# Optimization experiments

Hardware: AMD Instinct MI355X
Metric: run time of the kernel (lower is better)

## Reference

```python
import jax, jax.numpy as jnp
import numpy as np

K = 4          # conv kernel size
DIL = 3        # conv dilation
EPS = 1e-5     # rms eps inside gate kernel
NORM_EPS = 1e-5  # RMSNorm eps for value rms


def setup_inputs() -> dict:
    key = jax.random.key(0)
    ks = jax.random.split(key, 10)
    B, T, G, C, E = 2, 4096, 4, 1024, 1024
    return {
        "embeddings": jax.random.normal(ks[0], (B, T, E), jnp.float32),
        "hidden_states": jax.random.normal(ks[1], (B, T, G, C), jnp.float32),
        "key_w": jax.random.normal(ks[2], (G * C, E), jnp.float32) * 0.02,
        "key_b": jax.random.normal(ks[3], (G * C,), jnp.float32) * 0.02,
        "value_w": jax.random.normal(ks[4], (C, E), jnp.float32) * 0.02,
        "value_b": jax.random.normal(ks[5], (C,), jnp.float32) * 0.02,
        "w_key_norm": jax.random.uniform(ks[6], (G, C), jnp.float32, 0.5, 1.5),
        "w_query_norm": jax.random.uniform(ks[7], (G, C), jnp.float32, 0.5, 1.5),
        "w_norm": jax.random.uniform(ks[8], (G, C), jnp.float32, 0.5, 1.5),
        "conv_weight": jax.random.normal(ks[9], (G * C, K), jnp.float32) * 0.1,
    }


def reference(embeddings, hidden_states, key_w, key_b, value_w, value_b,
              w_key_norm, w_query_norm, w_norm, conv_weight):
    B, T, G, C = hidden_states.shape
    # projections
    k_all = (embeddings @ key_w.T + key_b).reshape(B, T, G, C)     # [B,T,G,C]
    q_all = hidden_states                                          # [B,T,G,C]
    vproj = embeddings @ value_w.T + value_b                       # [B,T,C]

    # gate kernel: per (b,t,g) RMS of key/query + weighted dot -> sign-sqrt-sigmoid gate
    rms_k = jnp.sqrt(jnp.mean(k_all * k_all, axis=-1) + EPS)       # [B,T,G]
    rms_q = jnp.sqrt(jnp.mean(q_all * q_all, axis=-1) + EPS)       # [B,T,G]
    dot = jnp.einsum('btgc,gc,btgc,gc->btg', k_all, w_key_norm, q_all, w_query_norm)
    gate_raw = dot / (rms_k * rms_q) / jnp.sqrt(jnp.float32(C))
    gate = jax.nn.sigmoid(jnp.where(gate_raw >= 0, 1.0, -1.0)
                          * jnp.sqrt(jnp.maximum(jnp.abs(gate_raw), 1e-6)))
    value = vproj[:, :, None, :] * gate[..., None]                 # [B,T,G,C]
    rms_v = jnp.sqrt(jnp.mean(value * value, axis=-1) + NORM_EPS)  # [B,T,G]

    # conv+residual kernel: per-group RMS-norm, dilated depthwise causal conv, SiLU, residual
    normed = value * (w_norm[None, None] / rms_v[..., None])       # [B,T,G,C]
    conv_w = conv_weight.reshape(G, C, K)                          # depthwise weights
    pad = (K - 1) * DIL
    xp = jnp.pad(normed, ((0, 0), (pad, 0), (0, 0), (0, 0)))
    # acc[b,t,g,c] = sum_k normed[b, t-(K-1-k)*DIL, g, c] * conv_w[g,c,k]
    acc = xp[:, 0:T] * conv_w[None, None, :, :, 0]
    for k in range(1, K):
        acc = acc + xp[:, k * DIL: k * DIL + T] * conv_w[None, None, :, :, k]
    acc = acc * jax.nn.sigmoid(acc)  # SiLU activation
    return value + acc
```

## Files before the change

### kernel.cpp

```cpp
#include <hip/hip_runtime.h>
#include <hip/hip_bf16.h>
#include <cstdint>
#include <cstddef>

using bf16 = __hip_bfloat16;

typedef __bf16 bf16x8_t __attribute__((ext_vector_type(8)));
typedef float  f32x4_t  __attribute__((ext_vector_type(4)));

static constexpr int Bb = 2;
static constexpr int Tt = 4096;
static constexpr int Gg = 4;
static constexpr int Cc = 1024;
static constexpr int Mm = Bb * Tt;
static constexpr int GC = Gg * Cc;

__device__ __forceinline__ float bfbits2f(unsigned u) {
  union { unsigned i; float f; } c; c.i = u << 16; return c.f;
}
__device__ __forceinline__ ushort f2bfbits(float v) {
  union { __hip_bfloat16 h; ushort u; } c; c.h = __float2bfloat16(v); return c.u;
}

__device__ __forceinline__ void store_val(bf16* p, float v)  { *p = __float2bfloat16(v); }
__device__ __forceinline__ void store_val(float* p, float v) { *p = v; }

__device__ __forceinline__ void gld_lds16(const ushort* g, ushort* l) {
  __builtin_amdgcn_global_load_lds(
      (const __attribute__((address_space(1))) void*)g,
      (__attribute__((address_space(3))) void*)l, 16, 0, 0);
}

__global__ __launch_bounds__(256)
void cvt_bf16(const float* __restrict__ in, ushort* __restrict__ out, int n4)
{
  const int i = blockIdx.x * 256 + threadIdx.x;
  if (i >= n4) return;
  const float4 v = ((const float4*)in)[i];
  ushort4 o;
  o.x = f2bfbits(v.x); o.y = f2bfbits(v.y);
  o.z = f2bfbits(v.z); o.w = f2bfbits(v.w);
  ((ushort4*)out)[i] = o;
}

__global__ __launch_bounds__(256)
void cvt_split(const float* __restrict__ in, ushort* __restrict__ hi,
               ushort* __restrict__ lo, int n4)
{
  const int i = blockIdx.x * 256 + threadIdx.x;
  if (i >= n4) return;
  const float4 v = ((const float4*)in)[i];
  ushort4 h, l;
  h.x = f2bfbits(v.x); l.x = f2bfbits(v.x - bfbits2f(h.x));
  h.y = f2bfbits(v.y); l.y = f2bfbits(v.y - bfbits2f(h.y));
  h.z = f2bfbits(v.z); l.z = f2bfbits(v.z - bfbits2f(h.z));
  h.w = f2bfbits(v.w); l.w = f2bfbits(v.w - bfbits2f(h.w));
  ((ushort4*)hi)[i] = h;
  ((ushort4*)lo)[i] = l;
}

__global__ __launch_bounds__(256, 4)
void gemm_key_fused(const ushort* __restrict__ embH, const ushort* __restrict__ embL,
                    const ushort* __restrict__ kwH,  const ushort* __restrict__ kwL,
                    const float* __restrict__ key_b, const float* __restrict__ hid,
                    const float* __restrict__ wkn,   const float* __restrict__ wqn,
                    float* __restrict__ k2_part, float* __restrict__ dot_part,
                    float* __restrict__ q2_part)
{
  constexpr int K = Cc;
  __shared__ __align__(16) ushort sA[128 * 64];
  __shared__ __align__(16) ushort sB[128 * 64];

  const int tid  = threadIdx.x;
  const int lane = tid & 63;
  const int wave = tid >> 6;
  const int wm   = wave & 1;
  const int wn   = wave >> 1;
  const int row0 = blockIdx.y * 128;
  const int col0 = blockIdx.x * 128;

  const int srow = tid >> 3;
  const int schk = (tid & 7) ^ (srow & 7);
  const ushort* aBase = (schk < 4) ? embH : embL;
  const ushort* bBase = (schk < 4) ? kwH  : kwL;
  const int selem = (schk & 3) * 8;
  const int wofs  = wave * 512;

  f32x4_t acc[4][4] = {};

  for (int kt = 0; kt < K; kt += 32) {
#pragma unroll
    for (int p = 0; p < 4; ++p) {
      gld_lds16(aBase + (size_t)(row0 + p * 32 + srow) * K + kt + selem,
                sA + p * 2048 + wofs);
      gld_lds16(bBase + (size_t)(col0 + p * 32 + srow) * K + kt + selem,
                sB + p * 2048 + wofs);
    }
    __syncthreads();

    const int cH = (lane >> 4) ^ (lane & 7);
    const int cL = cH ^ 4;

    bf16x8_t afH[4], afL[4], bfH[4], bfL[4];
#pragma unroll
    for (int mi = 0; mi < 4; ++mi) {
      const int r = wm * 64 + mi * 16 + (lane & 15);
      afH[mi] = *(const bf16x8_t*)(sA + r * 64 + cH * 8);
      afL[mi] = *(const bf16x8_t*)(sA + r * 64 + cL * 8);
    }
#pragma unroll
    for (int ni = 0; ni < 4; ++ni) {
      const int r = wn * 64 + ni * 16 + (lane & 15);
      bfH[ni] = *(const bf16x8_t*)(sB + r * 64 + cH * 8);
      bfL[ni] = *(const bf16x8_t*)(sB + r * 64 + cL * 8);
    }
#pragma unroll
    for (int mi = 0; mi < 4; ++mi)
#pragma unroll
      for (int ni = 0; ni < 4; ++ni) {
        acc[mi][ni] = __builtin_amdgcn_mfma_f32_16x16x32_bf16(
            afH[mi], bfH[ni], acc[mi][ni], 0, 0, 0);
        acc[mi][ni] = __builtin_amdgcn_mfma_f32_16x16x32_bf16(
            afH[mi], bfL[ni], acc[mi][ni], 0, 0, 0);
        acc[mi][ni] = __builtin_amdgcn_mfma_f32_16x16x32_bf16(
            afL[mi], bfH[ni], acc[mi][ni], 0, 0, 0);
      }
    __syncthreads();
  }

  const int lrow = lane >> 4;
  const int lcol = lane & 15;
  const int g    = col0 >> 10;

  float s2[4][4] = {};
  float su[4][4] = {};
  float sq[4][4] = {};

#pragma unroll
  for (int ni = 0; ni < 4; ++ni) {
    const int col = col0 + wn * 64 + ni * 16 + lcol;
    const float kb = key_b[col];
    const float ww = wkn[col] * wqn[col];
#pragma unroll
    for (int mi = 0; mi < 4; ++mi) {
      const int rowb = row0 + wm * 64 + mi * 16 + lrow * 4;
#pragma unroll
      for (int r = 0; r < 4; ++r) {
        const float q = hid[(size_t)(rowb + r) * GC + col];
        const float k = acc[mi][ni][r] + kb;
        s2[mi][r] += k * k;
        su[mi][r] += k * ww * q;
        sq[mi][r] += q * q;
      }
    }
  }
#pragma unroll
  for (int off = 1; off < 16; off <<= 1) {
#pragma unroll
    for (int mi = 0; mi < 4; ++mi)
#pragma unroll
      for (int r = 0; r < 4; ++r) {
        s2[mi][r] += __shfl_xor(s2[mi][r], off);
        su[mi][r] += __shfl_xor(su[mi][r], off);
        sq[mi][r] += __shfl_xor(sq[mi][r], off);
      }
  }
  if (lcol == 0) {
#pragma unroll
    for (int mi = 0; mi < 4; ++mi) {
      const int rowb = row0 + wm * 64 + mi * 16 + lrow * 4;
#pragma unroll
      for (int r = 0; r < 4; ++r) {
        atomicAdd(&k2_part[(rowb + r) * Gg + g],  s2[mi][r]);
        atomicAdd(&dot_part[(rowb + r) * Gg + g], su[mi][r]);
        atomicAdd(&q2_part[(rowb + r) * Gg + g],  sq[mi][r]);
      }
    }
  }
}

template <typename OutT>
__global__ __launch_bounds__(256, 4)
void gemm_bt(const ushort* __restrict__ A, const ushort* __restrict__ Bm,
             const float* __restrict__ bias, OutT* __restrict__ C,
             int M, int N, int K)
{
  __shared__ __align__(16) ushort sA[128 * 64];
  __shared__ __align__(16) ushort sB[128 * 64];

  const int tid  = threadIdx.x;
  const int lane = tid & 63;
  const int wave = tid >> 6;
  const int wm   = wave & 1;
  const int wn   = wave >> 1;
  const int row0 = blockIdx.y * 128;
  const int col0 = blockIdx.x * 128;

  const int srow = tid >> 3;
  const int scol = ((tid & 7) ^ (srow & 7)) * 8;
  ushort* aWB = sA + wave * 512;
  ushort* bWB = sB + wave * 512;

  f32x4_t acc[4][4] = {};

  for (int kt = 0; kt < K; kt += 64) {
#pragma unroll
    for (int p = 0; p < 4; ++p) {
      gld_lds16(A  + (size_t)(row0 + p * 32 + srow) * K + kt + scol,
                aWB + p * 2048);
      gld_lds16(Bm + (size_t)(col0 + p * 32 + srow) * K + kt + scol,
                bWB + p * 2048);
    }
    __syncthreads();

#pragma unroll
    for (int ks = 0; ks < 2; ++ks) {
      const int cb = ks * 4 + (lane >> 4);
      const int ce = ((cb ^ (lane & 7)) * 8);
      bf16x8_t af[4], bfr[4];
#pragma unroll
      for (int mi = 0; mi < 4; ++mi) {
        const int r = wm * 64 + mi * 16 + (lane & 15);
        af[mi] = *(const bf16x8_t*)(sA + r * 64 + ce);
      }
#pragma unroll
      for (int ni = 0; ni < 4; ++ni) {
        const int r = wn * 64 + ni * 16 + (lane & 15);
        bfr[ni] = *(const bf16x8_t*)(sB + r * 64 + ce);
      }
#pragma unroll
      for (int mi = 0; mi < 4; ++mi)
#pragma unroll
        for (int ni = 0; ni < 4; ++ni)
          acc[mi][ni] = __builtin_amdgcn_mfma_f32_16x16x32_bf16(
              af[mi], bfr[ni], acc[mi][ni], 0, 0, 0);
    }
    __syncthreads();
  }

  const int lrow = lane >> 4;
  const int lcol = lane & 15;
#pragma unroll
  for (int ni = 0; ni < 4; ++ni) {
    const int col = col0 + wn * 64 + ni * 16 + lcol;
    const float bv = bias[col];
#pragma unroll
    for (int mi = 0; mi < 4; ++mi) {
      const int rowb = row0 + wm * 64 + mi * 16 + lrow * 4;
#pragma unroll
      for (int r = 0; r < 4; ++r)
        store_val(&C[(size_t)(rowb + r) * N + col], acc[mi][ni][r] + bv);
    }
  }
}

__global__ __launch_bounds__(256)
void finalize_kernel(const float* __restrict__ vproj,
                     const float* __restrict__ k2_part,
                     const float* __restrict__ dot_part,
                     const float* __restrict__ q2_part,
                     float* __restrict__ gate_o, float* __restrict__ snorm_o)
{
  const int bt   = blockIdx.x;
  const int tid  = threadIdx.x;
  const int g    = tid >> 6;
  const int lane = tid & 63;

  const float4 v4 = ((const float4*)(vproj + (size_t)bt * Cc))[tid];
  float pv = v4.x * v4.x + v4.y * v4.y + v4.z * v4.z + v4.w * v4.w;
#pragma unroll
  for (int off = 32; off > 0; off >>= 1) pv += __shfl_xor(pv, off);
  __shared__ float wsum[4];
  if (lane == 0) wsum[g] = pv;
  __syncthreads();

  if (lane == 0) {
    const float mv = (wsum[0] + wsum[1] + wsum[2] + wsum[3]) * (1.0f / 1024.0f);
    const float sk = k2_part[bt * Gg + g];
    const float sd = dot_part[bt * Gg + g];
    const float sq = q2_part[bt * Gg + g];
    const float rk = sqrtf(sk * (1.0f / 1024.0f) + 1e-5f);
    const float rq = sqrtf(sq * (1.0f / 1024.0f) + 1e-5f);
    const float graw = sd / (rk * rq) * (1.0f / 32.0f);
    const float sgn = (graw >= 0.f) ? 1.f : -1.f;
    const float gate = 1.f / (1.f + expf(-sgn * sqrtf(fmaxf(fabsf(graw), 1e-6f))));
    const float rv = sqrtf(gate * gate * mv + 1e-5f);
    gate_o[bt * Gg + g]  = gate;
    snorm_o[bt * Gg + g] = gate / rv;
  }
}

static constexpr int CJ  = 128;
static constexpr int NCH = 11;

__global__ __launch_bounds__(256)
void conv_kernel(const float* __restrict__ vproj, const float* __restrict__ gate,
                 const float* __restrict__ snorm, const float* __restrict__ wnm,
                 const float* __restrict__ cw, float* __restrict__ out)
{
  int x = blockIdx.x;
  const int cb = x & 3;  x >>= 2;
  const int p  = x % 3;  x /= 3;
  const int ch = x % NCH; x /= NCH;
  const int g  = x & 3;  x >>= 2;
  const int b  = x;
  const int c  = cb * 256 + threadIdx.x;

  const float wn = wnm[g * Cc + c];
  const float4 w = ((const float4*)cw)[g * Cc + c];

  int t = p + 3 * (ch * CJ);
  if (t >= Tt) return;

  float n1 = 0.f, n2 = 0.f, n3 = 0.f;
#pragma unroll
  for (int h = 3; h >= 1; --h) {
    const int th = t - 3 * h;
    float nv = 0.f;
    if (th >= 0) {
      const int bt = b * Tt + th;
      nv = vproj[(size_t)bt * Cc + c] * snorm[bt * Gg + g] * wn;
    }
    n3 = n2; n2 = n1; n1 = nv;
  }

  for (int j = 0; j < CJ && t < Tt; ++j, t += 3) {
    const int bt = b * Tt + t;
    const float vp  = vproj[(size_t)bt * Cc + c];
    const float gt  = gate[bt * Gg + g];
    const float sn  = snorm[bt * Gg + g];
    const float cur = vp * sn * wn;
    const float a   = w.x * n3 + w.y * n2 + w.z * n1 + w.w * cur;
    const float si  = a / (1.f + __expf(-a));
    out[((size_t)bt * Gg + g) * Cc + c] = vp * gt + si;
    n3 = n2; n2 = n1; n1 = cur;
  }
}

extern "C" void kernel_launch(void* const* d_in, const int* in_sizes, int n_in,
                              void* d_out, int out_size, void* d_ws, size_t ws_size,
                              hipStream_t stream)
{
  const float* emb   = (const float*)d_in[0];
  const float* hid   = (const float*)d_in[1];
  const float* key_w = (const float*)d_in[2];
  const float* key_b = (const float*)d_in[3];
  const float* val_w = (const float*)d_in[4];
  const float* val_b = (const float*)d_in[5];
  const float* wkn   = (const float*)d_in[6];
  const float* wqn   = (const float*)d_in[7];
  const float* wnm   = (const float*)d_in[8];
  const float* cwt   = (const float*)d_in[9];
  float* out = (float*)d_out;

  char* ws = (char*)d_ws;
  ushort* embH  = (ushort*)ws;  ws += (size_t)Mm * Cc * 2;
  ushort* embL  = (ushort*)ws;  ws += (size_t)Mm * Cc * 2;
  ushort* kwH   = (ushort*)ws;  ws += (size_t)GC * Cc * 2;
  ushort* kwL   = (ushort*)ws;  ws += (size_t)GC * Cc * 2;
  ushort* vwB   = (ushort*)ws;  ws += (size_t)Cc * Cc * 2;
  float*  vproj = (float*)ws;   ws += (size_t)Mm * Cc * 4;
  float*  k2p   = (float*)ws;   ws += (size_t)Mm * Gg * 4;
  float*  dotp  = (float*)ws;   ws += (size_t)Mm * Gg * 4;
  float*  q2p   = (float*)ws;   ws += (size_t)Mm * Gg * 4;
  float*  gate  = (float*)ws;   ws += (size_t)Mm * Gg * 4;
  float*  snorm = (float*)ws;

  hipMemsetAsync(k2p, 0, (size_t)3 * Mm * Gg * 4, stream);

  dim3 blk(256);
  cvt_split<<<dim3((Mm * Cc / 4) / 256), blk, 0, stream>>>(emb,   embH, embL, Mm * Cc / 4);
  cvt_split<<<dim3((GC * Cc / 4) / 256), blk, 0, stream>>>(key_w, kwH,  kwL,  GC * Cc / 4);
  cvt_bf16 <<<dim3((Cc * Cc / 4) / 256), blk, 0, stream>>>(val_w, vwB,  Cc * Cc / 4);

  gemm_key_fused<<<dim3(GC / 128, Mm / 128), blk, 0, stream>>>(
      embH, embL, kwH, kwL, key_b, hid, wkn, wqn, k2p, dotp, q2p);

  gemm_bt<float><<<dim3(Cc / 128, Mm / 128), blk, 0, stream>>>(
      embH, vwB, val_b, vproj, Mm, Cc, Cc);

  finalize_kernel<<<dim3(Mm), blk, 0, stream>>>(vproj, k2p, dotp, q2p, gate, snorm);

  const int nblocks = Bb * Gg * NCH * 3 * (Cc / 256);
  conv_kernel<<<dim3(nblocks), blk, 0, stream>>>(vproj, gate, snorm, wnm, cwt, out);
}
```

Baseline: 615.5 us.

## Restructure key GEMM into 256x256 tiles with double-buffered ping-pong pipeline

```diff
diff --git a/kernel.cpp b/kernel.cpp
--- a/kernel.cpp
+++ b/kernel.cpp
@@ -59,7 +59,7 @@
   ((ushort4*)lo)[i] = l;
 }
 
-__global__ __launch_bounds__(256, 4)
+__global__ __launch_bounds__(512, 2)
 void gemm_key_fused(const ushort* __restrict__ embH, const ushort* __restrict__ embL,
                     const ushort* __restrict__ kwH,  const ushort* __restrict__ kwL,
                     const float* __restrict__ key_b, const float* __restrict__ hid,
@@ -67,113 +67,141 @@
                     float* __restrict__ k2_part, float* __restrict__ dot_part,
                     float* __restrict__ q2_part)
 {
-  constexpr int K = Cc;
-  __shared__ __align__(16) ushort sA[128 * 64];
-  __shared__ __align__(16) ushort sB[128 * 64];
+  constexpr int NT = 32;
+  __shared__ __align__(16) ushort sA[2 * 16384];
+  __shared__ __align__(16) ushort sB[2 * 16384];
 
   const int tid  = threadIdx.x;
   const int lane = tid & 63;
   const int wave = tid >> 6;
   const int wm   = wave & 1;
   const int wn   = wave >> 1;
-  const int row0 = blockIdx.y * 128;
-  const int col0 = blockIdx.x * 128;
-
-  const int srow = tid >> 3;
-  const int schk = (tid & 7) ^ (srow & 7);
-  const ushort* aBase = (schk < 4) ? embH : embL;
-  const ushort* bBase = (schk < 4) ? kwH  : kwL;
-  const int selem = (schk & 3) * 8;
-  const int wofs  = wave * 512;
-
-  f32x4_t acc[4][4] = {};
-
-  for (int kt = 0; kt < K; kt += 32) {
-#pragma unroll
-    for (int p = 0; p < 4; ++p) {
-      gld_lds16(aBase + (size_t)(row0 + p * 32 + srow) * K + kt + selem,
-                sA + p * 2048 + wofs);
-      gld_lds16(bBase + (size_t)(col0 + p * 32 + srow) * K + kt + selem,
-                sB + p * 2048 + wofs);
-    }
-    __syncthreads();
-
-    const int cH = (lane >> 4) ^ (lane & 7);
-    const int cL = cH ^ 4;
-
-    bf16x8_t afH[4], afL[4], bfH[4], bfL[4];
-#pragma unroll
-    for (int mi = 0; mi < 4; ++mi) {
-      const int r = wm * 64 + mi * 16 + (lane & 15);
-      afH[mi] = *(const bf16x8_t*)(sA + r * 64 + cH * 8);
-      afL[mi] = *(const bf16x8_t*)(sA + r * 64 + cL * 8);
-    }
-#pragma unroll
-    for (int ni = 0; ni < 4; ++ni) {
-      const int r = wn * 64 + ni * 16 + (lane & 15);
-      bfH[ni] = *(const bf16x8_t*)(sB + r * 64 + cH * 8);
-      bfL[ni] = *(const bf16x8_t*)(sB + r * 64 + cL * 8);
-    }
-#pragma unroll
-    for (int mi = 0; mi < 4; ++mi)
-#pragma unroll
-      for (int ni = 0; ni < 4; ++ni) {
-        acc[mi][ni] = __builtin_amdgcn_mfma_f32_16x16x32_bf16(
-            afH[mi], bfH[ni], acc[mi][ni], 0, 0, 0);
-        acc[mi][ni] = __builtin_amdgcn_mfma_f32_16x16x32_bf16(
-            afH[mi], bfL[ni], acc[mi][ni], 0, 0, 0);
-        acc[mi][ni] = __builtin_amdgcn_mfma_f32_16x16x32_bf16(
-            afL[mi], bfH[ni], acc[mi][ni], 0, 0, 0);
-      }
-    __syncthreads();
-  }
+  const int l15  = lane & 15;
+  const int cH   = (lane >> 4) ^ (lane & 7);
+  const int row0 = blockIdx.y * 256;
+  const int col0 = blockIdx.x * 256;
+
+  const int sRow = tid >> 3;
+  const int schk = (tid & 7) ^ (sRow & 7);
+  const ushort* aSel = (schk < 4) ? embH : embL;
+  const ushort* bSel = (schk < 4) ? kwH  : kwL;
+  const int sel8 = (schk & 3) * 8;
+  const int wofs = wave * 512;
+
+  auto stageA = [&](int rb, int u, int b) {
+    const size_t co = (size_t)u * 32 + sel8;
+    gld_lds16(aSel + (size_t)(row0 + rb + sRow) * Cc + co,
+              sA + b * 16384 + (rb >> 6) * 4096 + wofs);
+    gld_lds16(aSel + (size_t)(row0 + rb + 64 + sRow) * Cc + co,
+              sA + b * 16384 + ((rb >> 6) + 1) * 4096 + wofs);
+  };
+  auto stageB = [&](int rb, int u, int b) {
+    const size_t co = (size_t)u * 32 + sel8;
+    gld_lds16(bSel + (size_t)(col0 + rb + sRow) * Cc + co,
+              sB + b * 16384 + (rb >> 6) * 4096 + wofs);
+    gld_lds16(bSel + (size_t)(col0 + rb + 64 + sRow) * Cc + co,
+              sB + b * 16384 + ((rb >> 6) + 1) * 4096 + wofs);
+  };
+
+  f32x4_t acc[2][2][4][2] = {};
+
+#define PHASE(QM, QN, STAGE, DOVM)                                          \
+  {                                                                         \
+    bf16x8_t afH[4], afL[4], bgH[2], bgL[2];                                \
+    _Pragma("unroll") for (int mi = 0; mi < 4; ++mi) {                      \
+      const int r = (QM) * 128 + wm * 64 + mi * 16 + l15;                   \
+      const ushort* pa = bufA + r * 64;                                     \
+      afH[mi] = *(const bf16x8_t*)(pa + cH * 8);                            \
+      afL[mi] = *(const bf16x8_t*)(pa + (cH ^ 4) * 8);                      \
+    }                                                                       \
+    _Pragma("unroll") for (int ni = 0; ni < 2; ++ni) {                      \
+      const int r = (QN) * 128 + wn * 32 + ni * 16 + l15;                   \
+      const ushort* pb = bufB + r * 64;                                     \
+      bgH[ni] = *(const bf16x8_t*)(pb + cH * 8);                            \
+      bgL[ni] = *(const bf16x8_t*)(pb + (cH ^ 4) * 8);                      \
+    }                                                                       \
+    STAGE;                                                                  \
+    asm volatile("s_barrier" ::: "memory");                                 \
+    asm volatile("s_waitcnt lgkmcnt(0)" ::: "memory");                      \
+    __builtin_amdgcn_s_setprio(1);                                          \
+    _Pragma("unroll") for (int mi = 0; mi < 4; ++mi)                        \
+      _Pragma("unroll") for (int ni = 0; ni < 2; ++ni) {                    \
+        acc[QM][QN][mi][ni] = __builtin_amdgcn_mfma_f32_16x16x32_bf16(      \
+            afH[mi], bgH[ni], acc[QM][QN][mi][ni], 0, 0, 0);                \
+        acc[QM][QN][mi][ni] = __builtin_amdgcn_mfma_f32_16x16x32_bf16(      \
+            afH[mi], bgL[ni], acc[QM][QN][mi][ni], 0, 0, 0);                \
+        acc[QM][QN][mi][ni] = __builtin_amdgcn_mfma_f32_16x16x32_bf16(      \
+            afL[mi], bgH[ni], acc[QM][QN][mi][ni], 0, 0, 0);                \
+      }                                                                     \
+    __builtin_amdgcn_s_setprio(0);                                          \
+    if (DOVM) { asm volatile("s_waitcnt vmcnt(4)" ::: "memory"); }          \
+    asm volatile("s_barrier" ::: "memory");                                 \
+  }
+
+  stageA(0, 0, 0); stageB(0, 0, 0); stageB(128, 0, 0); stageA(128, 0, 0);
+  asm volatile("s_waitcnt vmcnt(4)" ::: "memory");
+  asm volatile("s_barrier" ::: "memory");
+
+  for (int u = 0; u < NT; ++u) {
+    const int b = u & 1, nb = b ^ 1;
+    const ushort* bufA = sA + b * 16384;
+    const ushort* bufB = sB + b * 16384;
+    const bool pf = (u + 1 < NT);
+    PHASE(0, 0, if (pf) stageA(0, u + 1, nb),   1)
+    PHASE(0, 1, if (pf) stageB(0, u + 1, nb),   1)
+    PHASE(1, 0, if (pf) stageB(128, u + 1, nb), 0)
+    PHASE(1, 1, if (pf) stageA(128, u + 1, nb), 1)
+  }
+#undef PHASE
 
   const int lrow = lane >> 4;
   const int lcol = lane & 15;
   const int g    = col0 >> 10;
 
-  float s2[4][4] = {};
-  float su[4][4] = {};
-  float sq[4][4] = {};
-
-#pragma unroll
-  for (int ni = 0; ni < 4; ++ni) {
-    const int col = col0 + wn * 64 + ni * 16 + lcol;
-    const float kb = key_b[col];
-    const float ww = wkn[col] * wqn[col];
-#pragma unroll
-    for (int mi = 0; mi < 4; ++mi) {
-      const int rowb = row0 + wm * 64 + mi * 16 + lrow * 4;
-#pragma unroll
-      for (int r = 0; r < 4; ++r) {
-        const float q = hid[(size_t)(rowb + r) * GC + col];
-        const float k = acc[mi][ni][r] + kb;
-        s2[mi][r] += k * k;
-        su[mi][r] += k * ww * q;
-        sq[mi][r] += q * q;
+#pragma unroll
+  for (int qm = 0; qm < 2; ++qm) {
+    float s2[4][4] = {}, su[4][4] = {}, sq[4][4] = {};
+#pragma unroll
+    for (int qn = 0; qn < 2; ++qn)
+#pragma unroll
+      for (int ni = 0; ni < 2; ++ni) {
+        const int col = col0 + qn * 128 + wn * 32 + ni * 16 + lcol;
+        const float kb = key_b[col];
+        const float ww = wkn[col] * wqn[col];
+#pragma unroll
+        for (int mi = 0; mi < 4; ++mi) {
+          const int rowb = row0 + qm * 128 + wm * 64 + mi * 16 + lrow * 4;
+#pragma unroll
+          for (int r = 0; r < 4; ++r) {
+            const float q = hid[(size_t)(rowb + r) * GC + col];
+            const float k = acc[qm][qn][mi][ni][r] + kb;
+            s2[mi][r] += k * k;
+            su[mi][r] += k * ww * q;
+            sq[mi][r] += q * q;
+          }
+        }
       }
-    }
-  }
-#pragma unroll
-  for (int off = 1; off < 16; off <<= 1) {
-#pragma unroll
-    for (int mi = 0; mi < 4; ++mi)
-#pragma unroll
-      for (int r = 0; r < 4; ++r) {
-        s2[mi][r] += __shfl_xor(s2[mi][r], off);
-        su[mi][r] += __shfl_xor(su[mi][r], off);
-        sq[mi][r] += __shfl_xor(sq[mi][r], off);
-      }
-  }
-  if (lcol == 0) {
-#pragma unroll
-    for (int mi = 0; mi < 4; ++mi) {
-      const int rowb = row0 + wm * 64 + mi * 16 + lrow * 4;
-#pragma unroll
-      for (int r = 0; r < 4; ++r) {
-        atomicAdd(&k2_part[(rowb + r) * Gg + g],  s2[mi][r]);
-        atomicAdd(&dot_part[(rowb + r) * Gg + g], su[mi][r]);
-        atomicAdd(&q2_part[(rowb + r) * Gg + g],  sq[mi][r]);
+#pragma unroll
+    for (int off = 1; off < 16; off <<= 1) {
+#pragma unroll
+      for (int mi = 0; mi < 4; ++mi)
+#pragma unroll
+        for (int r = 0; r < 4; ++r) {
+          s2[mi][r] += __shfl_xor(s2[mi][r], off);
+          su[mi][r] += __shfl_xor(su[mi][r], off);
+          sq[mi][r] += __shfl_xor(sq[mi][r], off);
+        }
+    }
+    if (lcol == 0) {
+#pragma unroll
+      for (int mi = 0; mi < 4; ++mi) {
+        const int rowb = row0 + qm * 128 + wm * 64 + mi * 16 + lrow * 4;
+#pragma unroll
+        for (int r = 0; r < 4; ++r) {
+          atomicAdd(&k2_part[(rowb + r) * Gg + g],  s2[mi][r]);
+          atomicAdd(&dot_part[(rowb + r) * Gg + g], su[mi][r]);
+          atomicAdd(&q2_part[(rowb + r) * Gg + g],  sq[mi][r]);
+        }
       }
     }
   }
@@ -373,7 +401,7 @@
   cvt_split<<<dim3((GC * Cc / 4) / 256), blk, 0, stream>>>(key_w, kwH,  kwL,  GC * Cc / 4);
   cvt_bf16 <<<dim3((Cc * Cc / 4) / 256), blk, 0, stream>>>(val_w, vwB,  Cc * Cc / 4);
 
-  gemm_key_fused<<<dim3(GC / 128, Mm / 128), blk, 0, stream>>>(
+  gemm_key_fused<<<dim3(GC / 256, Mm / 256), dim3(512), 0, stream>>>(
       embH, embL, kwH, kwL, key_b, hid, wkn, wqn, k2p, dotp, q2p);
 
   gemm_bt<float><<<dim3(Cc / 128, Mm / 128), blk, 0, stream>>>(
```

New measurement: 588.7 us. 1.05x faster.
